# Optimization experiments

Measured on AMD Instinct MI355X. Metric: run time of the kernel, lower is better.

## Reference

```python
import jax, jax.numpy as jnp
import numpy as np

B, S, HID = 2, 2048, 2048
NH, HD, RD = 16, 128, 64
KVC, QC = 512, 1536


def _apply_rope(t):
    # t: [B, H, S, R]; standard half-split rotary embedding
    R = t.shape[-1]
    s = t.shape[-2]
    inv_freq = 1.0 / (10000.0 ** (jnp.arange(0, R, 2, dtype=jnp.float32) / R))  # [R/2]
    ang = jnp.arange(s, dtype=jnp.float32)[:, None] * inv_freq[None, :]  # [S, R/2]
    cos, sin = jnp.cos(ang), jnp.sin(ang)
    t1, t2 = t[..., : R // 2], t[..., R // 2 :]
    return jnp.concatenate([t1 * cos - t2 * sin, t2 * cos + t1 * sin], axis=-1)


def setup_inputs() -> dict:
    key = jax.random.key(0)
    ks = jax.random.split(key, 20)

    def lin(k, fan_in, fan_out):
        bound = 1.0 / np.sqrt(fan_in)
        kw, kb = jax.random.split(k)
        W = jax.random.uniform(kw, (fan_in, fan_out), jnp.float32, -bound, bound)
        b = jax.random.uniform(kb, (fan_out,), jnp.float32, -bound, bound)
        return W, b

    x = jax.random.normal(ks[0], (B, S, HID), jnp.float32)
    W_kvd, b_kvd = lin(ks[1], HID, KVC)
    W_ku, b_ku = lin(ks[2], KVC, NH * HD)
    W_vu, b_vu = lin(ks[3], KVC, NH * HD)
    W_kr, b_kr = lin(ks[4], KVC, NH * RD)
    W_qd, b_qd = lin(ks[5], HID, QC)
    W_qu, b_qu = lin(ks[6], QC, NH * HD)
    W_qr, b_qr = lin(ks[7], QC, NH * RD)
    W_o, b_o = lin(ks[8], NH * HD, HID)
    return dict(x=x, W_kvd=W_kvd, b_kvd=b_kvd, W_ku=W_ku, b_ku=b_ku,
                W_vu=W_vu, b_vu=b_vu, W_kr=W_kr, b_kr=b_kr,
                W_qd=W_qd, b_qd=b_qd, W_qu=W_qu, b_qu=b_qu,
                W_qr=W_qr, b_qr=b_qr, W_o=W_o, b_o=b_o)


def reference(x, W_kvd, b_kvd, W_ku, b_ku, W_vu, b_vu, W_kr, b_kr,
              W_qd, b_qd, W_qu, b_qu, W_qr, b_qr, W_o, b_o):
    b, s, _ = x.shape

    def heads(t, d):  # [B,S,NH*d] -> [B,NH,S,d]
        return t.reshape(b, s, NH, d).transpose(0, 2, 1, 3)

    kv_c = x @ W_kvd + b_kvd                     # [B,S,KVC]
    keys_c = heads(kv_c @ W_ku + b_ku, HD)       # [B,H,S,HD]
    values = heads(kv_c @ W_vu + b_vu, HD)
    keys_r = _apply_rope(heads(kv_c @ W_kr + b_kr, RD))

    q_c = x @ W_qd + b_qd                        # [B,S,QC]
    queries_c = heads(q_c @ W_qu + b_qu, HD)
    queries_r = _apply_rope(heads(q_c @ W_qr + b_qr, RD))

    q = jnp.concatenate([queries_c, queries_r], axis=-1)  # [B,H,S,HD+RD]
    k = jnp.concatenate([keys_c, keys_r], axis=-1)

    scale = 1.0 / np.sqrt(HD + RD)
    scores = jnp.einsum('bhqd,bhkd->bhqk', q, k) * scale
    causal = jnp.triu(jnp.ones((s, s), dtype=bool), k=1)
    scores = jnp.where(causal[None, None], jnp.float32(-1e9), scores)
    probs = jax.nn.softmax(scores, axis=-1)
    ctx = jnp.einsum('bhqk,bhkd->bhqd', probs, values)    # [B,H,S,HD]
    ctx = ctx.transpose(0, 2, 1, 3).reshape(b, s, NH * HD)
    return ctx @ W_o + b_o
```

## Files before the change

kernel.cpp:

```cpp
#include <hip/hip_runtime.h>
#include <math.h>

#define BB   2
#define SS   2048
#define HIDD 2048
#define NHH  16
#define HDD  128
#define RDD  64
#define KVCC 512
#define QCC  1536
#define DQK  192
#define MROWS 4096

using bf16x8 = __attribute__((ext_vector_type(8))) short;
using short4v = __attribute__((ext_vector_type(4))) short;
using f32x4  = __attribute__((ext_vector_type(4))) float;
using f32x16 = __attribute__((ext_vector_type(16))) float;

static __device__ __forceinline__ float b2f(short s) {
    unsigned u = ((unsigned)(unsigned short)s) << 16;
    union { unsigned u; float f; } v; v.u = u; return v.f;
}
static __device__ __forceinline__ short f2b(float f) {
    union { float f; unsigned u; } v; v.f = f;
    unsigned r = (v.u + 0x7fffu + ((v.u >> 16) & 1u)) >> 16;
    return (short)r;
}
static __device__ __forceinline__ unsigned cvtpk(float lo, float hi) {
    unsigned r;
    asm("v_cvt_pk_bf16_f32 %0, %1, %2" : "=v"(r) : "v"(lo), "v"(hi));
    return r;
}

#define GLOAD16(gsrc, ldst) \
    __builtin_amdgcn_global_load_lds((const __attribute__((address_space(1))) void*)(gsrc), \
                                     (__attribute__((address_space(3))) void*)(ldst), 16, 0, 0)

__global__ void cvt_kernel(const float* __restrict__ in, short* __restrict__ out) {
    int i = (blockIdx.x * blockDim.x + threadIdx.x) * 4;
    float4 v = *(const float4*)(in + i);
    short4v o;
    o[0] = f2b(v.x); o[1] = f2b(v.y); o[2] = f2b(v.z); o[3] = f2b(v.w);
    *(short4v*)(out + i) = o;
}

__global__ void wtrans_kernel(
    const float* __restrict__ W0, const float* __restrict__ W1,
    const float* __restrict__ W2, const float* __restrict__ W3,
    const float* __restrict__ W4, const float* __restrict__ W5,
    const float* __restrict__ W6, const float* __restrict__ W7,
    short* __restrict__ D0, short* __restrict__ D1,
    short* __restrict__ D2, short* __restrict__ D3) {
    __shared__ float t[32][33];
    int bid = blockIdx.x;
    const float* W; short* Dst; int K, N, lt;
    if (bid < 4096) {
        if (bid < 1024) { W = W0; Dst = D0;                        K = 2048; N = 512;  lt = bid; }
        else            { W = W1; Dst = D0 + (size_t)512 * 2048;   K = 2048; N = 1536; lt = bid - 1024; }
    } else if (bid < 6656) {
        if (bid < 5120)      { W = W2; Dst = D1;                       K = 512; N = 2048; lt = bid - 4096; }
        else if (bid < 6144) { W = W3; Dst = D1 + (size_t)2048 * 512;  K = 512; N = 2048; lt = bid - 5120; }
        else                 { W = W4; Dst = D1 + (size_t)4096 * 512;  K = 512; N = 1024; lt = bid - 6144; }
    } else if (bid < 11264) {
        if (bid < 9728) { W = W5; Dst = D2;                        K = 1536; N = 2048; lt = bid - 6656; }
        else            { W = W6; Dst = D2 + (size_t)2048 * 1536;  K = 1536; N = 1024; lt = bid - 9728; }
    } else { W = W7; Dst = D3; K = 2048; N = 2048; lt = bid - 11264; }
    int ntx = N >> 5;
    int n0 = (lt % ntx) * 32, k0 = (lt / ntx) * 32;
    int tx = threadIdx.x, ty = threadIdx.y;
#pragma unroll
    for (int i = 0; i < 4; i++)
        t[ty + i * 8][tx] = W[(size_t)(k0 + ty + i * 8) * N + n0 + tx];
    __syncthreads();
#pragma unroll
    for (int i = 0; i < 4; i++)
        Dst[(size_t)(n0 + ty + i * 8) * K + k0 + tx] = f2b(t[tx][ty + i * 8]);
}

template <int ID>
__global__ __launch_bounds__(256) void gemm128(
    const short* __restrict__ A, const short* __restrict__ Bt,
    const float* __restrict__ b0, const float* __restrict__ b1, const float* __restrict__ b2,
    void* __restrict__ C0, void* __restrict__ C1,
    int M, int N, int K) {
    __shared__ short Asm[4096];
    __shared__ short Bsm[4096];
    int tid = threadIdx.x, lane = tid & 63, w = tid >> 6;
    int wm = w >> 1, wn = w & 1;
    int m0 = blockIdx.y * 128, n0 = blockIdx.x * 128;
    int fr = lane & 15, fk = (lane >> 4) * 8;
    const short* Ag = A + (size_t)(m0 + (tid >> 2)) * K + (tid & 3) * 8;
    const short* Bg = Bt + (size_t)(n0 + (tid >> 2)) * K + (tid & 3) * 8;
    f32x4 acc[4][4] = {};
    for (int k0 = 0; k0 < K; k0 += 32) {
        __syncthreads();
        GLOAD16(Ag + k0, &Asm[tid * 8]);
        GLOAD16(Ag + k0 + (size_t)64 * K, &Asm[2048 + tid * 8]);
        GLOAD16(Bg + k0, &Bsm[tid * 8]);
        GLOAD16(Bg + k0 + (size_t)64 * K, &Bsm[2048 + tid * 8]);
        __syncthreads();
        bf16x8 af[4], bfv[4];
#pragma unroll
        for (int m = 0; m < 4; m++)
            af[m] = *(const bf16x8*)&Asm[(wm * 64 + m * 16 + fr) * 32 + fk];
#pragma unroll
        for (int n = 0; n < 4; n++)
            bfv[n] = *(const bf16x8*)&Bsm[(wn * 64 + n * 16 + fr) * 32 + fk];
#pragma unroll
        for (int m = 0; m < 4; m++)
#pragma unroll
            for (int n = 0; n < 4; n++)
                acc[m][n] = __builtin_amdgcn_mfma_f32_16x16x32_bf16(af[m], bfv[n], acc[m][n], 0, 0, 0);
    }
#pragma unroll
    for (int m = 0; m < 4; m++)
#pragma unroll
        for (int n = 0; n < 4; n++)
#pragma unroll
            for (int r = 0; r < 4; r++) {
                int row = m0 + wm * 64 + m * 16 + ((lane >> 4) << 2) + r;
                int col = n0 + wn * 64 + n * 16 + fr;
                float v = acc[m][n][r];
                if constexpr (ID == 0) {
                    ((float*)C0)[(size_t)row * N + col] = v + b0[col];
                } else if constexpr (ID == 1) {
                    if (col < KVCC)
                        ((short*)C0)[(size_t)row * KVCC + col] = f2b(v + b0[col]);
                    else
                        ((short*)C1)[(size_t)row * QCC + (col - KVCC)] = f2b(v + b1[col - KVCC]);
                } else if constexpr (ID == 2) {
                    int b = row >> 11, s = row & (SS - 1);
                    if (col < 2048) {
                        int h = col >> 7, d = col & 127;
                        ((short*)C0)[(((size_t)(b * NHH + h)) * SS + s) * DQK + d] = f2b(v + b0[col]);
                    } else if (col < 4096) {
                        int c = col - 2048; int h = c >> 7, d = c & 127;
                        ((short*)C1)[(((size_t)(b * NHH + h)) * HDD + d) * SS + s] = f2b(v + b1[c]);
                    } else {
                        int c = col - 4096; int h = c >> 6, d = c & 63;
                        ((short*)C0)[(((size_t)(b * NHH + h)) * SS + s) * DQK + HDD + d] = f2b(v + b2[c]);
                    }
                } else {
                    int b = row >> 11, s = row & (SS - 1);
                    if (col < 2048) {
                        int h = col >> 7, d = col & 127;
                        ((short*)C0)[(((size_t)(b * NHH + h)) * SS + s) * DQK + d] = f2b(v + b0[col]);
                    } else {
                        int c = col - 2048; int h = c >> 6, d = c & 63;
                        ((short*)C0)[(((size_t)(b * NHH + h)) * SS + s) * DQK + HDD + d] = f2b(v + b1[c]);
                    }
                }
            }
}

__global__ void rope_kernel(short* __restrict__ Tk, short* __restrict__ Tq) {
    int idx = blockIdx.x * blockDim.x + threadIdx.x;
    const int HALF = BB * NHH * SS * 32;
    short* T = (idx < HALF) ? Tk : Tq;
    int id = (idx < HALF) ? idx : idx - HALF;
    int i = id & 31;
    int s = (id >> 5) & (SS - 1);
    int bh = id >> 16;
    short* p = T + ((size_t)bh * SS + s) * DQK + HDD;
    float t1 = b2f(p[i]), t2 = b2f(p[i + 32]);
    float inv = exp2f(-(float)i * 0.41524101186092034f);
    float ang = (float)s * inv;
    float sn, cs;
    sincosf(ang, &sn, &cs);
    p[i] = f2b(t1 * cs - t2 * sn);
    p[i + 32] = f2b(t2 * cs + t1 * sn);
}

__global__ __launch_bounds__(256, 2) void attn_kernel(
    const short* __restrict__ Q, const short* __restrict__ Kg,
    const short* __restrict__ Vt, short* __restrict__ ctx) {
    __shared__ short Ksm[2][64 * 192];
    __shared__ short Vsm[2][128 * 64];
    int tid = threadIdx.x, lane = tid & 63, w = tid >> 6;
    int hf = lane >> 5, l31 = lane & 31;
    int bid = blockIdx.x;
    int half = bid >> 8, a = (bid & 255) >> 5;
    int qt = half ? a : 15 - a;
    int bh = bid & 31;
    int bb = bh >> 4, hd = bh & 15;
    int q0 = qt * 128;
    const short* Qp = Q + (size_t)bh * SS * DQK;
    const short* Kp = Kg + (size_t)bh * SS * DQK;
    const char*  Vp = (const char*)(Vt + (size_t)bh * HDD * SS);
    int wr0 = q0 + w * 32;
    int qrow = wr0 + l31;
    const float scale = 0.07216878364870323f;
    const float L2E = 1.44269504088896f;

    bf16x8 qf[12];
#pragma unroll
    for (int s = 0; s < 12; s++)
        qf[s] = *(const bf16x8*)(Qp + (size_t)qrow * DQK + s * 16 + hf * 8);

    f32x16 acc[4] = {};
    float mrow = -1e30f, lsum = 0.f;
    int nt = 2 * qt + 2;

    auto stageK = [&](int key0, int b) {
#pragma unroll
        for (int pp = 0; pp < 6; pp++) {
            int flat = pp * 4096 + tid * 16;
            int row = flat / 384, bir = flat - row * 384;
            const char* src = (const char*)Kp + (size_t)(key0 + row) * 384 + (bir ^ ((row & 7) << 4));
            GLOAD16(src, (char*)Ksm[b] + flat);
        }
    };
    auto stageV = [&](int key0, int b) {
#pragma unroll
        for (int c = 0; c < 4; c++) {
            int flat = c * 4096 + tid * 16;
            int d = flat >> 7, bik = flat & 127;
            const char* src = Vp + (size_t)d * (SS * 2) + (size_t)key0 * 2 + (bik ^ ((d & 7) << 4));
            GLOAD16(src, (char*)Vsm[b] + flat);
        }
    };

    stageK(0, 0); stageV(0, 0);
    __syncthreads();

    for (int t0 = 0; t0 < nt; t0++) {
        int key0 = t0 * 64;
        int cur = t0 & 1;
        if (t0 + 1 < nt) { stageK(key0 + 64, cur ^ 1); stageV(key0 + 64, cur ^ 1); }
        bool active = (key0 <= wr0 + 31);
        if (active) {
            f32x16 z = {};
            f32x16 sv0 = z, sv1 = z;
            int xr = (l31 & 7) << 4;
            const char* Kb = (const char*)Ksm[cur];
            __builtin_amdgcn_s_setprio(1);
#pragma unroll
            for (int s = 0; s < 12; s++) {
                bf16x8 k0 = *(const bf16x8*)(Kb + l31 * 384 + ((s * 32 + hf * 16) ^ xr));
                bf16x8 k1 = *(const bf16x8*)(Kb + (32 + l31) * 384 + ((s * 32 + hf * 16) ^ xr));
                sv0 = __builtin_amdgcn_mfma_f32_32x32x16_bf16(k0, qf[s], sv0, 0, 0, 0);
                sv1 = __builtin_amdgcn_mfma_f32_32x32x16_bf16(k1, qf[s], sv1, 0, 0, 0);
            }
            __builtin_amdgcn_s_setprio(0);
            bool domask = (key0 + 63 > wr0);
            float p[32];
#pragma unroll
            for (int t = 0; t < 2; t++)
#pragma unroll
                for (int r = 0; r < 16; r++) {
                    float v = (t ? sv1[r] : sv0[r]);
                    int key = key0 + 32 * t + (r & 3) + 8 * (r >> 2) + 4 * hf;
                    if (domask && key > qrow) v = -1e30f;
                    p[t * 16 + r] = v;
                }
            float tm[16];
#pragma unroll
            for (int i = 0; i < 16; i++) tm[i] = fmaxf(p[i], p[i + 16]);
#pragma unroll
            for (int i = 0; i < 8; i++) tm[i] = fmaxf(tm[i], tm[i + 8]);
#pragma unroll
            for (int i = 0; i < 4; i++) tm[i] = fmaxf(tm[i], tm[i + 4]);
            float pmaxs = fmaxf(fmaxf(tm[0], tm[1]), fmaxf(tm[2], tm[3])) * scale;
            if (__any(pmaxs > mrow + 8.f)) {
                float pc = fmaxf(pmaxs, __shfl_xor(pmaxs, 32, 64));
                float mn = fmaxf(mrow, pc);
                float al = exp2f((mrow - mn) * L2E);
                mrow = mn;
                lsum *= al;
                float arl[16];
#pragma unroll
                for (int r = 0; r < 16; r++)
                    arl[r] = __shfl(al, (r & 3) + 8 * (r >> 2) + 4 * hf, 64);
#pragma unroll
                for (int n = 0; n < 4; n++)
#pragma unroll
                    for (int r = 0; r < 16; r++)
                        acc[n][r] *= arl[r];
            }
            float sL = scale * L2E, mL = mrow * L2E;
#pragma unroll
            for (int i = 0; i < 32; i++)
                p[i] = exp2f(fmaf(p[i], sL, -mL));
            float ts[16];
#pragma unroll
            for (int i = 0; i < 16; i++) ts[i] = p[i] + p[i + 16];
#pragma unroll
            for (int i = 0; i < 8; i++) ts[i] = ts[i] + ts[i + 8];
#pragma unroll
            for (int i = 0; i < 4; i++) ts[i] = ts[i] + ts[i + 4];
            lsum += (ts[0] + ts[1]) + (ts[2] + ts[3]);
            bf16x8 afv[4];
#pragma unroll
            for (int g = 0; g < 4; g++) {
                int base = (g >> 1) * 16 + (g & 1) * 8;
                unsigned a01 = cvtpk(p[base + 0], p[base + 1]);
                unsigned a23 = cvtpk(p[base + 2], p[base + 3]);
                unsigned b01 = cvtpk(p[base + 4], p[base + 5]);
                unsigned b23 = cvtpk(p[base + 6], p[base + 7]);
                unsigned s0 = hf ? a01 : b01, s1 = hf ? a23 : b23;
                unsigned r0 = (unsigned)__shfl_xor((int)s0, 32, 64);
                unsigned r1 = (unsigned)__shfl_xor((int)s1, 32, 64);
                union { unsigned u[4]; bf16x8 v; } af;
                af.u[0] = hf ? r0 : a01;
                af.u[1] = hf ? r1 : a23;
                af.u[2] = hf ? b01 : r0;
                af.u[3] = hf ? b23 : r1;
                afv[g] = af.v;
            }
            const char* Vb = (const char*)Vsm[cur];
            __builtin_amdgcn_s_setprio(1);
#pragma unroll
            for (int g = 0; g < 4; g++)
#pragma unroll
                for (int n = 0; n < 4; n++) {
                    int d = n * 32 + l31;
                    bf16x8 vf = *(const bf16x8*)(Vb + d * 128 + ((g * 32 + hf * 16) ^ ((d & 7) << 4)));
                    acc[n] = __builtin_amdgcn_mfma_f32_32x32x16_bf16(afv[g], vf, acc[n], 0, 0, 0);
                }
            __builtin_amdgcn_s_setprio(0);
        }
        __syncthreads();
    }
    lsum += __shfl_xor(lsum, 32, 64);
    float rc = 1.0f / lsum;
    float rcl[16];
#pragma unroll
    for (int r = 0; r < 16; r++)
        rcl[r] = __shfl(rc, (r & 3) + 8 * (r >> 2) + 4 * hf, 64);
#pragma unroll
    for (int n = 0; n < 4; n++)
#pragma unroll
        for (int r = 0; r < 16; r++) {
            int row = wr0 + (r & 3) + 8 * (r >> 2) + 4 * hf;
            int d = n * 32 + l31;
            ctx[((size_t)(bb * SS + row)) * (NHH * HDD) + hd * HDD + d] = f2b(acc[n][r] * rcl[r]);
        }
}

extern "C" void kernel_launch(void* const* d_in, const int* in_sizes, int n_in,
                              void* d_out, int out_size, void* d_ws, size_t ws_size,
                              hipStream_t stream) {
    const float* x     = (const float*)d_in[0];
    const float* W_kvd = (const float*)d_in[1];  const float* b_kvd = (const float*)d_in[2];
    const float* W_ku  = (const float*)d_in[3];  const float* b_ku  = (const float*)d_in[4];
    const float* W_vu  = (const float*)d_in[5];  const float* b_vu  = (const float*)d_in[6];
    const float* W_kr  = (const float*)d_in[7];  const float* b_kr  = (const float*)d_in[8];
    const float* W_qd  = (const float*)d_in[9];  const float* b_qd  = (const float*)d_in[10];
    const float* W_qu  = (const float*)d_in[11]; const float* b_qu  = (const float*)d_in[12];
    const float* W_qr  = (const float*)d_in[13]; const float* b_qr  = (const float*)d_in[14];
    const float* W_o   = (const float*)d_in[15]; const float* b_o   = (const float*)d_in[16];
    float* out = (float*)d_out;

    char* p = (char*)d_ws;
    auto alloc = [&](size_t elems) {
        short* r = (short*)p;
        p += ((elems * 2) + 255) & ~(size_t)255;
        return r;
    };
    short* xb   = alloc((size_t)MROWS * HIDD);
    short* kvc  = alloc((size_t)MROWS * KVCC);
    short* qc   = alloc((size_t)MROWS * QCC);
    short* kbuf = alloc((size_t)BB * NHH * SS * DQK);
    short* qbuf = alloc((size_t)BB * NHH * SS * DQK);
    short* vtb  = alloc((size_t)BB * NHH * HDD * SS);
    short* ctx  = alloc((size_t)MROWS * NHH * HDD);
    short* Wt1  = alloc((size_t)2048 * 2048);
    short* Wt2  = alloc((size_t)5120 * 512);
    short* Wt3  = alloc((size_t)3072 * 1536);
    short* Wt4  = alloc((size_t)2048 * 2048);

    cvt_kernel<<<dim3((MROWS * HIDD) / 1024), dim3(256), 0, stream>>>(x, xb);
    dim3 tb(32, 8);
    wtrans_kernel<<<dim3(15360), tb, 0, stream>>>(
        W_kvd, W_qd, W_ku, W_vu, W_kr, W_qu, W_qr, W_o, Wt1, Wt2, Wt3, Wt4);

    gemm128<1><<<dim3(2048 / 128, MROWS / 128), 256, 0, stream>>>(
        xb, Wt1, b_kvd, b_qd, nullptr, kvc, qc, MROWS, 2048, 2048);
    gemm128<2><<<dim3(5120 / 128, MROWS / 128), 256, 0, stream>>>(
        kvc, Wt2, b_ku, b_vu, b_kr, kbuf, vtb, MROWS, 5120, 512);
    gemm128<3><<<dim3(3072 / 128, MROWS / 128), 256, 0, stream>>>(
        qc, Wt3, b_qu, b_qr, nullptr, qbuf, nullptr, MROWS, 3072, 1536);

    rope_kernel<<<dim3((2 * BB * NHH * SS * 32) / 256), dim3(256), 0, stream>>>(kbuf, qbuf);

    attn_kernel<<<dim3(512), 256, 0, stream>>>(qbuf, kbuf, vtb, ctx);

    gemm128<0><<<dim3(HIDD / 128, MROWS / 128), 256, 0, stream>>>(
        ctx, Wt4, b_o, nullptr, nullptr, out, nullptr, MROWS, HIDD, NHH * HDD);
}
```

Baseline: 403.0 us.

## Balance causal attention work by splitting long query tiles across two blocks

Pairs each short query tile with the first part of a long one, so every block processes the same number of key tiles. Long query tiles are computed in two halves that write unnormalized partial outputs plus max and sum stats into reused workspace. A new merge kernel combines the halves. This removes the causal load imbalance at the cost of extra partial-output traffic and an additional kernel launch.

```diff
diff --git a/kernel.cpp b/kernel.cpp
--- a/kernel.cpp
+++ b/kernel.cpp
@@ -173,33 +173,23 @@
 
 __global__ __launch_bounds__(256, 2) void attn_kernel(
     const short* __restrict__ Q, const short* __restrict__ Kg,
-    const short* __restrict__ Vt, short* __restrict__ ctx) {
+    const short* __restrict__ Vt, short* __restrict__ ctx,
+    float* __restrict__ Opart, float* __restrict__ Ml) {
     __shared__ short Ksm[2][64 * 192];
     __shared__ short Vsm[2][128 * 64];
     int tid = threadIdx.x, lane = tid & 63, w = tid >> 6;
     int hf = lane >> 5, l31 = lane & 31;
     int bid = blockIdx.x;
-    int half = bid >> 8, a = (bid & 255) >> 5;
-    int qt = half ? a : 15 - a;
-    int bh = bid & 31;
+    int bh = bid & 31, slot = bid >> 5;
+    int pa = slot & 7, role = slot >> 3;
+    int lo = pa, hi = 15 - pa;
+    int c = 15 - 2 * pa;
     int bb = bh >> 4, hd = bh & 15;
-    int q0 = qt * 128;
     const short* Qp = Q + (size_t)bh * SS * DQK;
     const short* Kp = Kg + (size_t)bh * SS * DQK;
     const char*  Vp = (const char*)(Vt + (size_t)bh * HDD * SS);
-    int wr0 = q0 + w * 32;
-    int qrow = wr0 + l31;
     const float scale = 0.07216878364870323f;
     const float L2E = 1.44269504088896f;
-
-    bf16x8 qf[12];
-#pragma unroll
-    for (int s = 0; s < 12; s++)
-        qf[s] = *(const bf16x8*)(Qp + (size_t)qrow * DQK + s * 16 + hf * 8);
-
-    f32x16 acc[4] = {};
-    float mrow = -1e30f, lsum = 0.f;
-    int nt = 2 * qt + 2;
 
     auto stageK = [&](int key0, int b) {
 #pragma unroll
@@ -212,129 +202,200 @@
     };
     auto stageV = [&](int key0, int b) {
 #pragma unroll
-        for (int c = 0; c < 4; c++) {
-            int flat = c * 4096 + tid * 16;
+        for (int cc = 0; cc < 4; cc++) {
+            int flat = cc * 4096 + tid * 16;
             int d = flat >> 7, bik = flat & 127;
             const char* src = Vp + (size_t)d * (SS * 2) + (size_t)key0 * 2 + (bik ^ ((d & 7) << 4));
             GLOAD16(src, (char*)Vsm[b] + flat);
         }
     };
 
-    stageK(0, 0); stageV(0, 0);
-    __syncthreads();
-
-    for (int t0 = 0; t0 < nt; t0++) {
-        int key0 = t0 * 64;
-        int cur = t0 & 1;
-        if (t0 + 1 < nt) { stageK(key0 + 64, cur ^ 1); stageV(key0 + 64, cur ^ 1); }
-        bool active = (key0 <= wr0 + 31);
-        if (active) {
-            f32x16 z = {};
-            f32x16 sv0 = z, sv1 = z;
-            int xr = (l31 & 7) << 4;
-            const char* Kb = (const char*)Ksm[cur];
-            __builtin_amdgcn_s_setprio(1);
-#pragma unroll
-            for (int s = 0; s < 12; s++) {
-                bf16x8 k0 = *(const bf16x8*)(Kb + l31 * 384 + ((s * 32 + hf * 16) ^ xr));
-                bf16x8 k1 = *(const bf16x8*)(Kb + (32 + l31) * 384 + ((s * 32 + hf * 16) ^ xr));
-                sv0 = __builtin_amdgcn_mfma_f32_32x32x16_bf16(k0, qf[s], sv0, 0, 0, 0);
-                sv1 = __builtin_amdgcn_mfma_f32_32x32x16_bf16(k1, qf[s], sv1, 0, 0, 0);
+    int nseg = (role == 0) ? 2 : 1;
+    for (int sg = 0; sg < nseg; sg++) {
+        int qt_, kb, ke, mode;
+        if (role == 0) {
+            if (sg == 0) { qt_ = lo; kb = 0; ke = 2 * lo + 2; mode = 0; }
+            else         { qt_ = hi; kb = 0; ke = c;          mode = 1; }
+        } else          { qt_ = hi; kb = c; ke = 2 * hi + 2;  mode = 2; }
+        int q0 = qt_ * 128;
+        int wr0 = q0 + w * 32;
+        int qrow = wr0 + l31;
+        bf16x8 qf[12];
+#pragma unroll
+        for (int s = 0; s < 12; s++)
+            qf[s] = *(const bf16x8*)(Qp + (size_t)qrow * DQK + s * 16 + hf * 8);
+        f32x16 acc[4] = {};
+        float mrow = -1e30f, lsum = 0.f;
+
+        stageK(kb * 64, 0); stageV(kb * 64, 0);
+        __syncthreads();
+
+        for (int t = kb; t < ke; t++) {
+            int key0 = t * 64;
+            int cur = (t - kb) & 1;
+            if (t + 1 < ke) { stageK(key0 + 64, cur ^ 1); stageV(key0 + 64, cur ^ 1); }
+            bool active = (key0 <= wr0 + 31);
+            if (active) {
+                f32x16 z = {};
+                f32x16 sv0 = z, sv1 = z;
+                int xr = (l31 & 7) << 4;
+                const char* Kb = (const char*)Ksm[cur];
+                __builtin_amdgcn_s_setprio(1);
+#pragma unroll
+                for (int s = 0; s < 12; s++) {
+                    bf16x8 k0 = *(const bf16x8*)(Kb + l31 * 384 + ((s * 32 + hf * 16) ^ xr));
+                    bf16x8 k1 = *(const bf16x8*)(Kb + (32 + l31) * 384 + ((s * 32 + hf * 16) ^ xr));
+                    sv0 = __builtin_amdgcn_mfma_f32_32x32x16_bf16(k0, qf[s], sv0, 0, 0, 0);
+                    sv1 = __builtin_amdgcn_mfma_f32_32x32x16_bf16(k1, qf[s], sv1, 0, 0, 0);
+                }
+                __builtin_amdgcn_s_setprio(0);
+                bool domask = (key0 + 63 > wr0);
+                float p[32];
+#pragma unroll
+                for (int t2 = 0; t2 < 2; t2++)
+#pragma unroll
+                    for (int r = 0; r < 16; r++) {
+                        float v = (t2 ? sv1[r] : sv0[r]);
+                        int key = key0 + 32 * t2 + (r & 3) + 8 * (r >> 2) + 4 * hf;
+                        if (domask && key > qrow) v = -1e30f;
+                        p[t2 * 16 + r] = v;
+                    }
+                float tm[16];
+#pragma unroll
+                for (int i = 0; i < 16; i++) tm[i] = fmaxf(p[i], p[i + 16]);
+#pragma unroll
+                for (int i = 0; i < 8; i++) tm[i] = fmaxf(tm[i], tm[i + 8]);
+#pragma unroll
+                for (int i = 0; i < 4; i++) tm[i] = fmaxf(tm[i], tm[i + 4]);
+                float pmaxs = fmaxf(fmaxf(tm[0], tm[1]), fmaxf(tm[2], tm[3])) * scale;
+                if (__any(pmaxs > mrow + 8.f)) {
+                    float pc = fmaxf(pmaxs, __shfl_xor(pmaxs, 32, 64));
+                    float mn = fmaxf(mrow, pc);
+                    float al = exp2f((mrow - mn) * L2E);
+                    mrow = mn;
+                    lsum *= al;
+                    float arl[16];
+#pragma unroll
+                    for (int r = 0; r < 16; r++)
+                        arl[r] = __shfl(al, (r & 3) + 8 * (r >> 2) + 4 * hf, 64);
+#pragma unroll
+                    for (int n = 0; n < 4; n++)
+#pragma unroll
+                        for (int r = 0; r < 16; r++)
+                            acc[n][r] *= arl[r];
+                }
+                float sL = scale * L2E, mL = mrow * L2E;
+#pragma unroll
+                for (int i = 0; i < 32; i++)
+                    p[i] = exp2f(fmaf(p[i], sL, -mL));
+                float ts[16];
+#pragma unroll
+                for (int i = 0; i < 16; i++) ts[i] = p[i] + p[i + 16];
+#pragma unroll
+                for (int i = 0; i < 8; i++) ts[i] = ts[i] + ts[i + 8];
+#pragma unroll
+                for (int i = 0; i < 4; i++) ts[i] = ts[i] + ts[i + 4];
+                lsum += (ts[0] + ts[1]) + (ts[2] + ts[3]);
+                bf16x8 afv[4];
+#pragma unroll
+                for (int g = 0; g < 4; g++) {
+                    int base = (g >> 1) * 16 + (g & 1) * 8;
+                    unsigned a01 = cvtpk(p[base + 0], p[base + 1]);
+                    unsigned a23 = cvtpk(p[base + 2], p[base + 3]);
+                    unsigned b01 = cvtpk(p[base + 4], p[base + 5]);
+                    unsigned b23 = cvtpk(p[base + 6], p[base + 7]);
+                    unsigned s0 = hf ? a01 : b01, s1 = hf ? a23 : b23;
+                    unsigned r0 = (unsigned)__shfl_xor((int)s0, 32, 64);
+                    unsigned r1 = (unsigned)__shfl_xor((int)s1, 32, 64);
+                    union { unsigned u[4]; bf16x8 v; } af;
+                    af.u[0] = hf ? r0 : a01;
+                    af.u[1] = hf ? r1 : a23;
+                    af.u[2] = hf ? b01 : r0;
+                    af.u[3] = hf ? b23 : r1;
+                    afv[g] = af.v;
+                }
+                const char* Vb = (const char*)Vsm[cur];
+                __builtin_amdgcn_s_setprio(1);
+#pragma unroll
+                for (int g = 0; g < 4; g++)
+#pragma unroll
+                    for (int n = 0; n < 4; n++) {
+                        int d = n * 32 + l31;
+                        bf16x8 vf = *(const bf16x8*)(Vb + d * 128 + ((g * 32 + hf * 16) ^ ((d & 7) << 4)));
+                        acc[n] = __builtin_amdgcn_mfma_f32_32x32x16_bf16(afv[g], vf, acc[n], 0, 0, 0);
+                    }
+                __builtin_amdgcn_s_setprio(0);
             }
-            __builtin_amdgcn_s_setprio(0);
-            bool domask = (key0 + 63 > wr0);
-            float p[32];
-#pragma unroll
-            for (int t = 0; t < 2; t++)
+            __syncthreads();
+        }
+        lsum += __shfl_xor(lsum, 32, 64);
+        if (mode == 0) {
+            float rc = 1.0f / lsum;
+            float rcl[16];
+#pragma unroll
+            for (int r = 0; r < 16; r++)
+                rcl[r] = __shfl(rc, (r & 3) + 8 * (r >> 2) + 4 * hf, 64);
+#pragma unroll
+            for (int n = 0; n < 4; n++)
 #pragma unroll
                 for (int r = 0; r < 16; r++) {
-                    float v = (t ? sv1[r] : sv0[r]);
-                    int key = key0 + 32 * t + (r & 3) + 8 * (r >> 2) + 4 * hf;
-                    if (domask && key > qrow) v = -1e30f;
-                    p[t * 16 + r] = v;
-                }
-            float tm[16];
-#pragma unroll
-            for (int i = 0; i < 16; i++) tm[i] = fmaxf(p[i], p[i + 16]);
-#pragma unroll
-            for (int i = 0; i < 8; i++) tm[i] = fmaxf(tm[i], tm[i + 8]);
-#pragma unroll
-            for (int i = 0; i < 4; i++) tm[i] = fmaxf(tm[i], tm[i + 4]);
-            float pmaxs = fmaxf(fmaxf(tm[0], tm[1]), fmaxf(tm[2], tm[3])) * scale;
-            if (__any(pmaxs > mrow + 8.f)) {
-                float pc = fmaxf(pmaxs, __shfl_xor(pmaxs, 32, 64));
-                float mn = fmaxf(mrow, pc);
-                float al = exp2f((mrow - mn) * L2E);
-                mrow = mn;
-                lsum *= al;
-                float arl[16];
-#pragma unroll
-                for (int r = 0; r < 16; r++)
-                    arl[r] = __shfl(al, (r & 3) + 8 * (r >> 2) + 4 * hf, 64);
-#pragma unroll
-                for (int n = 0; n < 4; n++)
-#pragma unroll
-                    for (int r = 0; r < 16; r++)
-                        acc[n][r] *= arl[r];
+                    int row = wr0 + (r & 3) + 8 * (r >> 2) + 4 * hf;
+                    int d = n * 32 + l31;
+                    ctx[((size_t)(bb * SS + row)) * (NHH * HDD) + hd * HDD + d] = f2b(acc[n][r] * rcl[r]);
+                }
+        } else {
+            int si = bh * 8 + pa;
+            float* Op = Opart + ((size_t)si * 2 + (mode - 1)) * 16384;
+            float* mlp = Ml + ((size_t)si * 2 + (mode - 1)) * 256;
+#pragma unroll
+            for (int n = 0; n < 4; n++)
+#pragma unroll
+                for (int r = 0; r < 16; r++) {
+                    int row = w * 32 + (r & 3) + 8 * (r >> 2) + 4 * hf;
+                    Op[row * 128 + n * 32 + l31] = acc[n][r];
+                }
+            if (hf == 0) {
+                int row = w * 32 + l31;
+                mlp[row * 2] = mrow;
+                mlp[row * 2 + 1] = lsum;
             }
-            float sL = scale * L2E, mL = mrow * L2E;
-#pragma unroll
-            for (int i = 0; i < 32; i++)
-                p[i] = exp2f(fmaf(p[i], sL, -mL));
-            float ts[16];
-#pragma unroll
-            for (int i = 0; i < 16; i++) ts[i] = p[i] + p[i + 16];
-#pragma unroll
-            for (int i = 0; i < 8; i++) ts[i] = ts[i] + ts[i + 8];
-#pragma unroll
-            for (int i = 0; i < 4; i++) ts[i] = ts[i] + ts[i + 4];
-            lsum += (ts[0] + ts[1]) + (ts[2] + ts[3]);
-            bf16x8 afv[4];
-#pragma unroll
-            for (int g = 0; g < 4; g++) {
-                int base = (g >> 1) * 16 + (g & 1) * 8;
-                unsigned a01 = cvtpk(p[base + 0], p[base + 1]);
-                unsigned a23 = cvtpk(p[base + 2], p[base + 3]);
-                unsigned b01 = cvtpk(p[base + 4], p[base + 5]);
-                unsigned b23 = cvtpk(p[base + 6], p[base + 7]);
-                unsigned s0 = hf ? a01 : b01, s1 = hf ? a23 : b23;
-                unsigned r0 = (unsigned)__shfl_xor((int)s0, 32, 64);
-                unsigned r1 = (unsigned)__shfl_xor((int)s1, 32, 64);
-                union { unsigned u[4]; bf16x8 v; } af;
-                af.u[0] = hf ? r0 : a01;
-                af.u[1] = hf ? r1 : a23;
-                af.u[2] = hf ? b01 : r0;
-                af.u[3] = hf ? b23 : r1;
-                afv[g] = af.v;
-            }
-            const char* Vb = (const char*)Vsm[cur];
-            __builtin_amdgcn_s_setprio(1);
-#pragma unroll
-            for (int g = 0; g < 4; g++)
-#pragma unroll
-                for (int n = 0; n < 4; n++) {
-                    int d = n * 32 + l31;
-                    bf16x8 vf = *(const bf16x8*)(Vb + d * 128 + ((g * 32 + hf * 16) ^ ((d & 7) << 4)));
-                    acc[n] = __builtin_amdgcn_mfma_f32_32x32x16_bf16(afv[g], vf, acc[n], 0, 0, 0);
-                }
-            __builtin_amdgcn_s_setprio(0);
         }
-        __syncthreads();
     }
-    lsum += __shfl_xor(lsum, 32, 64);
-    float rc = 1.0f / lsum;
-    float rcl[16];
-#pragma unroll
-    for (int r = 0; r < 16; r++)
-        rcl[r] = __shfl(rc, (r & 3) + 8 * (r >> 2) + 4 * hf, 64);
-#pragma unroll
-    for (int n = 0; n < 4; n++)
-#pragma unroll
-        for (int r = 0; r < 16; r++) {
-            int row = wr0 + (r & 3) + 8 * (r >> 2) + 4 * hf;
-            int d = n * 32 + l31;
-            ctx[((size_t)(bb * SS + row)) * (NHH * HDD) + hd * HDD + d] = f2b(acc[n][r] * rcl[r]);
-        }
+}
+
+__global__ __launch_bounds__(256) void merge_kernel(
+    const float* __restrict__ Opart, const float* __restrict__ Ml,
+    short* __restrict__ ctx) {
+    int si = blockIdx.x;
+    int bh = si >> 3, pa = si & 7;
+    int hi = 15 - pa;
+    int q0 = hi * 128;
+    int bb = bh >> 4, hd = bh & 15;
+    const float* Oa = Opart + (size_t)si * 2 * 16384;
+    const float* Ob = Oa + 16384;
+    const float* mla = Ml + (size_t)si * 2 * 256;
+    const float* mlb = mla + 256;
+    int tid = threadIdx.x;
+    int rr = tid >> 5, dq = (tid & 31) * 4;
+    const float L2E = 1.44269504088896f;
+#pragma unroll
+    for (int it = 0; it < 16; it++) {
+        int row = it * 8 + rr;
+        float mA = mla[row * 2], lA = mla[row * 2 + 1];
+        float mB = mlb[row * 2], lB = mlb[row * 2 + 1];
+        float M = fmaxf(mA, mB);
+        float wA = exp2f((mA - M) * L2E), wB = exp2f((mB - M) * L2E);
+        float rc = 1.0f / (lA * wA + lB * wB);
+        float4 oa = *(const float4*)(Oa + row * 128 + dq);
+        float4 ob = *(const float4*)(Ob + row * 128 + dq);
+        size_t o = ((size_t)(bb * SS + q0 + row)) * (NHH * HDD) + hd * HDD + dq;
+        short4v r;
+        r[0] = f2b((oa.x * wA + ob.x * wB) * rc);
+        r[1] = f2b((oa.y * wA + ob.y * wB) * rc);
+        r[2] = f2b((oa.z * wA + ob.z * wB) * rc);
+        r[3] = f2b((oa.w * wA + ob.w * wB) * rc);
+        *(short4v*)(ctx + o) = r;
+    }
 }
 
 extern "C" void kernel_launch(void* const* d_in, const int* in_sizes, int n_in,
@@ -369,6 +430,9 @@
     short* Wt3  = alloc((size_t)3072 * 1536);
     short* Wt4  = alloc((size_t)2048 * 2048);
 
+    float* Opart = (float*)xb;
+    float* Ml    = (float*)Wt1;
+
     cvt_kernel<<<dim3((MROWS * HIDD) / 1024), dim3(256), 0, stream>>>(x, xb);
     dim3 tb(32, 8);
     wtrans_kernel<<<dim3(15360), tb, 0, stream>>>(
@@ -383,7 +447,8 @@
 
     rope_kernel<<<dim3((2 * BB * NHH * SS * 32) / 256), dim3(256), 0, stream>>>(kbuf, qbuf);
 
-    attn_kernel<<<dim3(512), 256, 0, stream>>>(qbuf, kbuf, vtb, ctx);
+    attn_kernel<<<dim3(512), 256, 0, stream>>>(qbuf, kbuf, vtb, ctx, Opart, Ml);
+    merge_kernel<<<dim3(256), 256, 0, stream>>>(Opart, Ml, ctx);
 
     gemm128<0><<<dim3(HIDD / 128, MROWS / 128), 256, 0, stream>>>(
         ctx, Wt4, b_o, nullptr, nullptr, out, nullptr, MROWS, HIDD, NHH * HDD);
```

After: 449.6 us. 1.12x slower.
